# Optimization experiments

Measured on AMD Instinct MI355X. Metric: run time of the kernel, lower is better.

## Reference

```python
import jax, jax.numpy as jnp
import numpy as np
from jax import lax

GRID_SIZE = 5
SPLINE_ORDER = 3
N_COEF = GRID_SIZE + SPLINE_ORDER  # 8 b-spline basis functions per input
GRID_LO, GRID_HI = -1.0, 1.0


def _grid():
    h = (GRID_HI - GRID_LO) / GRID_SIZE
    return jnp.arange(-SPLINE_ORDER, GRID_SIZE + SPLINE_ORDER + 1, dtype=jnp.float32) * h + GRID_LO


def _bsplines(x):
    # x: [..., in] -> [..., in, N_COEF] via Cox-de Boor recursion (efficient-kan)
    grid = _grid()
    x = x[..., None]
    bases = ((x >= grid[:-1]) & (x < grid[1:])).astype(x.dtype)
    for j in range(1, SPLINE_ORDER + 1):
        bases = ((x - grid[:-(j + 1)]) / (grid[j:-1] - grid[:-(j + 1)]) * bases[..., :-1]
                 + (grid[j + 1:] - x) / (grid[j + 1:] - grid[1:-j]) * bases[..., 1:])
    return bases


def _kan_linear(x, base_w, spline_w):
    # x: [..., in]; base_w: [out, in]; spline_w: [out, in, N_COEF]
    base = jax.nn.silu(x) @ base_w.T
    b = _bsplines(x).reshape(x.shape[:-1] + (-1,))  # [..., in*N_COEF]
    return base + b @ spline_w.reshape(spline_w.shape[0], -1).T


def _kan_conv(x, base_w, spline_w):
    # x: [B, C, H, W]; 3x3 valid KAN convolution
    patches = lax.conv_general_dilated_patches(x, (3, 3), (1, 1), 'VALID')  # [B, C*9, H-2, W-2]
    p = patches.transpose(0, 2, 3, 1)  # [B, Ho, Wo, C*9]
    out = _kan_linear(p, base_w, spline_w)  # [B, Ho, Wo, out]
    return out.transpose(0, 3, 1, 2)


def _maxpool2(x):
    return lax.reduce_window(x, -jnp.inf, lax.max, (1, 1, 2, 2), (1, 1, 2, 2), 'VALID')


def setup_inputs() -> dict:
    key = jax.random.key(0)
    ks = jax.random.split(key, 12)
    B = 2048
    x = jax.random.uniform(ks[0], (B, 1, 28, 28), dtype=jnp.float32)
    s = 0.1
    return {
        'x': x,
        'bw1': jax.random.normal(ks[1], (5, 9), dtype=jnp.float32) * s,
        'sw1': jax.random.normal(ks[2], (5, 9, N_COEF), dtype=jnp.float32) * s,
        'bw2': jax.random.normal(ks[3], (5, 45), dtype=jnp.float32) * s,
        'sw2': jax.random.normal(ks[4], (5, 45, N_COEF), dtype=jnp.float32) * s,
        'bw3': jax.random.normal(ks[5], (2, 45), dtype=jnp.float32) * s,
        'sw3': jax.random.normal(ks[6], (2, 45, N_COEF), dtype=jnp.float32) * s,
        'w1': jax.random.normal(ks[7], (500, 162), dtype=jnp.float32) * 0.05,
        'b1': jnp.zeros((500,), dtype=jnp.float32),
        'w2': jax.random.normal(ks[8], (10, 500), dtype=jnp.float32) * 0.05,
        'b2': jnp.zeros((10,), dtype=jnp.float32),
    }


def reference(x, bw1, sw1, bw2, sw2, bw3, sw3, w1, b1, w2, b2):
    h = _kan_conv(x, bw1, sw1)       # [B, 5, 26, 26]
    h = _maxpool2(h)                 # [B, 5, 13, 13]
    h = _kan_conv(h, bw2, sw2)       # [B, 5, 11, 11]
    h = _kan_conv(h, bw3, sw3)       # [B, 2, 9, 9]
    h = h.reshape(h.shape[0], -1)    # [B, 162]
    h = jax.nn.relu(h @ w1.T + b1)   # [B, 500]
    return h @ w2.T + b2             # [B, 10]
```

## Files before the change

### kernel.cpp

```cpp
#include <hip/hip_runtime.h>


typedef _Float16 h2 __attribute__((ext_vector_type(2)));

__device__ __forceinline__ h2 u2h(unsigned int u) {
  union { unsigned int x; h2 h; } v; v.x = u; return v.h;
}
__device__ __forceinline__ unsigned short f2h_bits(float x) {
  union { _Float16 h; unsigned short u; } v; v.h = (_Float16)x; return v.u;
}
__device__ __forceinline__ unsigned int pack2h(float a, float b) {
  return (unsigned int)f2h_bits(a) | ((unsigned int)f2h_bits(b) << 16);
}
__device__ __forceinline__ float fdot2(h2 a, h2 b, float c) {
  return __builtin_amdgcn_fdot2(a, b, c, false);
}

__device__ __forceinline__ void featurize_regs(float v, uint4& bs, float& silu) {
  silu = v / (1.0f + __expf(-v));
  bs.x = 0u; bs.y = 0u; bs.z = 0u; bs.w = 0u;
  float u = fmaf(v, 2.5f, 5.5f);
  if (u >= 0.0f && u < 11.0f) {
    float tf = floorf(u);
    float f = u - tf, f2 = f * f, f3 = f2 * f, om = 1.0f - f;
    const float c6 = 1.0f / 6.0f;
    float w0 = om * om * om * c6;
    float w1 = (3.0f * f3 - 6.0f * f2 + 4.0f) * c6;
    float w2 = (-3.0f * f3 + 3.0f * f2 + 3.0f * f + 1.0f) * c6;
    float w3 = f3 * c6;
    unsigned long long w01 =
        (unsigned long long)f2h_bits(w0) |
        ((unsigned long long)f2h_bits(w1) << 16) |
        ((unsigned long long)f2h_bits(w2) << 32) |
        ((unsigned long long)f2h_bits(w3) << 48);
    int t = (int)tf;
    int s = 16 * t - 48;
    unsigned long long lo, hi;
    if (s >= 0) {
      lo = (s < 64) ? (w01 << s) : 0ull;
      hi = (s == 0) ? 0ull : ((s < 64) ? (w01 >> (64 - s)) : (w01 << (s - 64)));
    } else {
      lo = w01 >> (-s);
      hi = 0ull;
    }
    bs.x = (unsigned int)lo; bs.y = (unsigned int)(lo >> 32);
    bs.z = (unsigned int)hi; bs.w = (unsigned int)(hi >> 32);
  }
}

__global__ __launch_bounds__(256) void k_prep(
    const float* __restrict__ bw1, const float* __restrict__ sw1,
    const float* __restrict__ bw2, const float* __restrict__ sw2,
    const float* __restrict__ bw3, const float* __restrict__ sw3,
    const float* __restrict__ w1,
    unsigned int* __restrict__ V1s, float* __restrict__ V1b,
    unsigned int* __restrict__ V2s, float* __restrict__ V2b,
    unsigned int* __restrict__ V3s, float* __restrict__ V3b,
    unsigned int* __restrict__ W1p) {
  int t = blockIdx.x * 256 + threadIdx.x;
  if (t < 180) {
    int p = t & 3, o = (t >> 2) % 5, in = t / 20;
    V1s[t] = pack2h(sw1[(o * 9 + in) * 8 + 2 * p], sw1[(o * 9 + in) * 8 + 2 * p + 1]);
  }
  if (t < 45)  { int o = t % 5, in = t / 5; V1b[t] = bw1[o * 9 + in]; }
  if (t < 900) {
    int p = t & 3, o = (t >> 2) % 5, in = t / 20;
    V2s[t] = pack2h(sw2[(o * 45 + in) * 8 + 2 * p], sw2[(o * 45 + in) * 8 + 2 * p + 1]);
  }
  if (t < 225) { int o = t % 5, in = t / 5; V2b[t] = bw2[o * 45 + in]; }
  if (t < 360) {
    int p = t & 3, o = (t >> 2) & 1, in = t / 8;
    V3s[t] = pack2h(sw3[(o * 45 + in) * 8 + 2 * p], sw3[(o * 45 + in) * 8 + 2 * p + 1]);
  }
  if (t < 90)  { int o = t % 2, in = t / 2; V3b[t] = bw3[o * 45 + in]; }
  if (t < 81 * 512) {
    int kp = t >> 9, o = t & 511;
    W1p[t] = (o < 500) ? pack2h(w1[o * 162 + 2 * kp], w1[o * 162 + 2 * kp + 1]) : 0u;
  }
}

__global__ __launch_bounds__(256) void k_fused(
    const float* __restrict__ x,
    const unsigned int* __restrict__ V1s, const float* __restrict__ V1b,
    const unsigned int* __restrict__ V2s, const float* __restrict__ V2b,
    const unsigned int* __restrict__ V3s, const float* __restrict__ V3b,
    const unsigned int* __restrict__ W1p,
    const float* __restrict__ b1,
    const float* __restrict__ W2, const float* __restrict__ b2,
    float* __restrict__ out) {
  __shared__ uint4 bas[845];
  __shared__ float ext[845];
  __shared__ float hbuf[845];
  __shared__ unsigned int hpk[81];
  const int b = blockIdx.x;
  const int tid = threadIdx.x;

  for (int l = tid; l < 784; l += 256) {
    uint4 bs; float sl;
    featurize_regs(x[b * 784 + l], bs, sl);
    bas[l] = bs; ext[l] = sl;
  }
  __syncthreads();

  if (tid < 169) {
    int py = tid / 13, px = tid % 13;
    int r0 = py * 2, c0 = px * 2;
    float wacc[4][5];
    #pragma unroll
    for (int wi = 0; wi < 4; ++wi)
      #pragma unroll
      for (int o = 0; o < 5; ++o) wacc[wi][o] = 0.0f;
    #pragma unroll
    for (int r = 0; r < 4; ++r) {
      #pragma unroll
      for (int c = 0; c < 4; ++c) {
        uint4 q = bas[(r0 + r) * 28 + c0 + c];
        float sl = ext[(r0 + r) * 28 + c0 + c];
        h2 a0 = u2h(q.x), a1 = u2h(q.y), a2 = u2h(q.z), a3 = u2h(q.w);
        #pragma unroll
        for (int dy = 0; dy < 2; ++dy) {
          #pragma unroll
          for (int dx = 0; dx < 2; ++dx) {
            int ky = r - dy, kx = c - dx;
            if (ky >= 0 && ky < 3 && kx >= 0 && kx < 3) {
              const unsigned int* wp = V1s + (ky * 3 + kx) * 20;
              const float* bp = V1b + (ky * 3 + kx) * 5;
              #pragma unroll
              for (int o = 0; o < 5; ++o) {
                float acc = wacc[dy * 2 + dx][o];
                acc = fdot2(a0, u2h(wp[o * 4 + 0]), acc);
                acc = fdot2(a1, u2h(wp[o * 4 + 1]), acc);
                acc = fdot2(a2, u2h(wp[o * 4 + 2]), acc);
                acc = fdot2(a3, u2h(wp[o * 4 + 3]), acc);
                wacc[dy * 2 + dx][o] = fmaf(sl, bp[o], acc);
              }
            }
          }
        }
      }
    }
    #pragma unroll
    for (int o = 0; o < 5; ++o) {
      float m = fmaxf(fmaxf(wacc[0][o], wacc[1][o]), fmaxf(wacc[2][o], wacc[3][o]));
      hbuf[o * 169 + tid] = m;
    }
  }
  __syncthreads();

  for (int l = tid; l < 845; l += 256) {
    uint4 bs; float sl;
    featurize_regs(hbuf[l], bs, sl);
    bas[l] = bs; ext[l] = sl;
  }
  __syncthreads();

  if (tid < 121) {
    int y = tid / 11, xx = tid % 11;
    float acc[5] = {0.f, 0.f, 0.f, 0.f, 0.f};
    #pragma unroll 1
    for (int cky = 0; cky < 15; ++cky) {
      int c = cky / 3, ky = cky % 3;
      int base = c * 169 + (y + ky) * 13 + xx;
      #pragma unroll
      for (int kx = 0; kx < 3; ++kx) {
        uint4 q = bas[base + kx];
        float sl = ext[base + kx];
        h2 a0 = u2h(q.x), a1 = u2h(q.y), a2 = u2h(q.z), a3 = u2h(q.w);
        const unsigned int* wp = V2s + (cky * 3 + kx) * 20;
        const float* bp = V2b + (cky * 3 + kx) * 5;
        #pragma unroll
        for (int o = 0; o < 5; ++o) {
          float a = acc[o];
          a = fdot2(a0, u2h(wp[o * 4 + 0]), a);
          a = fdot2(a1, u2h(wp[o * 4 + 1]), a);
          a = fdot2(a2, u2h(wp[o * 4 + 2]), a);
          a = fdot2(a3, u2h(wp[o * 4 + 3]), a);
          acc[o] = fmaf(sl, bp[o], a);
        }
      }
    }
    #pragma unroll
    for (int o = 0; o < 5; ++o) hbuf[o * 121 + tid] = acc[o];
  }
  __syncthreads();

  for (int l = tid; l < 605; l += 256) {
    uint4 bs; float sl;
    featurize_regs(hbuf[l], bs, sl);
    bas[l] = bs; ext[l] = sl;
  }
  __syncthreads();

  if (tid < 81) {
    int y = tid / 9, xx = tid % 9;
    float acc[2] = {0.f, 0.f};
    #pragma unroll 1
    for (int cky = 0; cky < 15; ++cky) {
      int c = cky / 3, ky = cky % 3;
      int base = c * 121 + (y + ky) * 11 + xx;
      #pragma unroll
      for (int kx = 0; kx < 3; ++kx) {
        uint4 q = bas[base + kx];
        float sl = ext[base + kx];
        h2 a0 = u2h(q.x), a1 = u2h(q.y), a2 = u2h(q.z), a3 = u2h(q.w);
        const unsigned int* wp = V3s + (cky * 3 + kx) * 8;
        const float* bp = V3b + (cky * 3 + kx) * 2;
        #pragma unroll
        for (int o = 0; o < 2; ++o) {
          float a = acc[o];
          a = fdot2(a0, u2h(wp[o * 4 + 0]), a);
          a = fdot2(a1, u2h(wp[o * 4 + 1]), a);
          a = fdot2(a2, u2h(wp[o * 4 + 2]), a);
          a = fdot2(a3, u2h(wp[o * 4 + 3]), a);
          acc[o] = fmaf(sl, bp[o], a);
        }
      }
    }
    hbuf[tid] = acc[0];
    hbuf[81 + tid] = acc[1];
  }
  __syncthreads();

  if (tid < 81) hpk[tid] = pack2h(hbuf[2 * tid], hbuf[2 * tid + 1]);
  __syncthreads();

  if (tid < 250) {
    float a0 = 0.0f, a1 = 0.0f;
    #pragma unroll 4
    for (int kp = 0; kp < 81; ++kp) {
      h2 hk = u2h(hpk[kp]);
      uint2 wv = *(const uint2*)(W1p + kp * 512 + 2 * tid);
      a0 = fdot2(hk, u2h(wv.x), a0);
      a1 = fdot2(hk, u2h(wv.y), a1);
    }
    int o0 = 2 * tid, o1 = 2 * tid + 1;
    float v0 = a0 + b1[o0], v1 = a1 + b1[o1];
    hbuf[200 + o0] = v0 > 0.0f ? v0 : 0.0f;
    hbuf[200 + o1] = v1 > 0.0f ? v1 : 0.0f;
  }
  __syncthreads();

  if (tid < 160) {
    int o = tid >> 4, part = tid & 15;
    float s = 0.0f;
    #pragma unroll
    for (int j = 0; j < 8; ++j) {
      int k = part * 4 + j * 64;
      if (k <= 496) {
        float4 w = *(const float4*)&W2[o * 500 + k];
        float4 h = *(const float4*)&hbuf[200 + k];
        s += w.x * h.x + w.y * h.y + w.z * h.z + w.w * h.w;
      }
    }
    hbuf[tid] = s;
  }
  __syncthreads();

  if (tid < 10) {
    float s = 0.0f;
    #pragma unroll
    for (int p = 0; p < 16; ++p) s += hbuf[tid * 16 + p];
    out[b * 10 + tid] = s + b2[tid];
  }
}

extern "C" void kernel_launch(void* const* d_in, const int* in_sizes, int n_in,
                              void* d_out, int out_size, void* d_ws, size_t ws_size,
                              hipStream_t stream) {
  (void)in_sizes; (void)n_in; (void)out_size; (void)ws_size;
  const float* x   = (const float*)d_in[0];
  const float* bw1 = (const float*)d_in[1];
  const float* sw1 = (const float*)d_in[2];
  const float* bw2 = (const float*)d_in[3];
  const float* sw2 = (const float*)d_in[4];
  const float* bw3 = (const float*)d_in[5];
  const float* sw3 = (const float*)d_in[6];
  const float* w1  = (const float*)d_in[7];
  const float* b1  = (const float*)d_in[8];
  const float* w2  = (const float*)d_in[9];
  const float* b2  = (const float*)d_in[10];
  float* out = (float*)d_out;

  char* ws = (char*)d_ws;
  unsigned int* V1s = (unsigned int*)(ws);
  float*        V1b = (float*)(ws + 768);
  unsigned int* V2s = (unsigned int*)(ws + 1024);
  float*        V2b = (float*)(ws + 4672);
  unsigned int* V3s = (unsigned int*)(ws + 5632);
  float*        V3b = (float*)(ws + 7168);
  unsigned int* W1p = (unsigned int*)(ws + 7680);

  k_prep<<<162, 256, 0, stream>>>(bw1, sw1, bw2, sw2, bw3, sw3, w1,
                                  V1s, V1b, V2s, V2b, V3s, V3b, W1p);
  k_fused<<<2048, 256, 0, stream>>>(x, V1s, V1b, V2s, V2b, V3s, V3b, W1p,
                                    b1, w2, b2, out);
}
```

Measured before the change: 141.0 us.

## Rebalance conv stages: per-pixel conv1 with separate pool, split-K conv2/conv3 across waves

Conv1 now computes each of the 676 output pixels once, with all threads participating, and stores them as fp16 in scratch. A separate pass then max-pools and featurizes, replacing the old scheme where 169 threads each computed a 2x2 window with redundant loads. Conv2 and conv3 split the input-channel/ky reduction across two wave parities so more threads are active. Partial sums are combined through scratch during the following featurize/pack step. This costs extra shared memory, an fp16 rounding of conv1 outputs before pooling, and an additional reduction step.

```diff
diff --git a/kernel.cpp b/kernel.cpp
--- a/kernel.cpp
+++ b/kernel.cpp
@@ -90,10 +90,14 @@
     float* __restrict__ out) {
   __shared__ uint4 bas[845];
   __shared__ float ext[845];
-  __shared__ float hbuf[845];
-  __shared__ unsigned int hpk[81];
+  __shared__ float hbuf[700];
+  __shared__ float scratch[1690];
+  unsigned short* co  = (unsigned short*)scratch;
+  unsigned int*  co32 = (unsigned int*)scratch;
+  unsigned int*  hpk  = (unsigned int*)ext;
   const int b = blockIdx.x;
   const int tid = threadIdx.x;
+  const int wv = tid >> 6, lane = tid & 63;
 
   for (int l = tid; l < 784; l += 256) {
     uint4 bs; float sl;
@@ -102,72 +106,19 @@
   }
   __syncthreads();
 
-  if (tid < 169) {
-    int py = tid / 13, px = tid % 13;
-    int r0 = py * 2, c0 = px * 2;
-    float wacc[4][5];
+  for (int l = tid; l < 676; l += 256) {
+    int y = l / 26, xx = l % 26;
+    float acc[5] = {0.f, 0.f, 0.f, 0.f, 0.f};
     #pragma unroll
-    for (int wi = 0; wi < 4; ++wi)
-      #pragma unroll
-      for (int o = 0; o < 5; ++o) wacc[wi][o] = 0.0f;
-    #pragma unroll
-    for (int r = 0; r < 4; ++r) {
-      #pragma unroll
-      for (int c = 0; c < 4; ++c) {
-        uint4 q = bas[(r0 + r) * 28 + c0 + c];
-        float sl = ext[(r0 + r) * 28 + c0 + c];
-        h2 a0 = u2h(q.x), a1 = u2h(q.y), a2 = u2h(q.z), a3 = u2h(q.w);
-        #pragma unroll
-        for (int dy = 0; dy < 2; ++dy) {
-          #pragma unroll
-          for (int dx = 0; dx < 2; ++dx) {
-            int ky = r - dy, kx = c - dx;
-            if (ky >= 0 && ky < 3 && kx >= 0 && kx < 3) {
-              const unsigned int* wp = V1s + (ky * 3 + kx) * 20;
-              const float* bp = V1b + (ky * 3 + kx) * 5;
-              #pragma unroll
-              for (int o = 0; o < 5; ++o) {
-                float acc = wacc[dy * 2 + dx][o];
-                acc = fdot2(a0, u2h(wp[o * 4 + 0]), acc);
-                acc = fdot2(a1, u2h(wp[o * 4 + 1]), acc);
-                acc = fdot2(a2, u2h(wp[o * 4 + 2]), acc);
-                acc = fdot2(a3, u2h(wp[o * 4 + 3]), acc);
-                wacc[dy * 2 + dx][o] = fmaf(sl, bp[o], acc);
-              }
-            }
-          }
-        }
-      }
-    }
-    #pragma unroll
-    for (int o = 0; o < 5; ++o) {
-      float m = fmaxf(fmaxf(wacc[0][o], wacc[1][o]), fmaxf(wacc[2][o], wacc[3][o]));
-      hbuf[o * 169 + tid] = m;
-    }
-  }
-  __syncthreads();
-
-  for (int l = tid; l < 845; l += 256) {
-    uint4 bs; float sl;
-    featurize_regs(hbuf[l], bs, sl);
-    bas[l] = bs; ext[l] = sl;
-  }
-  __syncthreads();
-
-  if (tid < 121) {
-    int y = tid / 11, xx = tid % 11;
-    float acc[5] = {0.f, 0.f, 0.f, 0.f, 0.f};
-    #pragma unroll 1
-    for (int cky = 0; cky < 15; ++cky) {
-      int c = cky / 3, ky = cky % 3;
-      int base = c * 169 + (y + ky) * 13 + xx;
+    for (int ky = 0; ky < 3; ++ky) {
       #pragma unroll
       for (int kx = 0; kx < 3; ++kx) {
-        uint4 q = bas[base + kx];
-        float sl = ext[base + kx];
+        int r = (y + ky) * 28 + xx + kx;
+        uint4 q = bas[r];
+        float sl = ext[r];
         h2 a0 = u2h(q.x), a1 = u2h(q.y), a2 = u2h(q.z), a3 = u2h(q.w);
-        const unsigned int* wp = V2s + (cky * 3 + kx) * 20;
-        const float* bp = V2b + (cky * 3 + kx) * 5;
+        const unsigned int* wp = V1s + (ky * 3 + kx) * 20;
+        const float* bp = V1b + (ky * 3 + kx) * 5;
         #pragma unroll
         for (int o = 0; o < 5; ++o) {
           float a = acc[o];
@@ -180,48 +131,106 @@
       }
     }
     #pragma unroll
-    for (int o = 0; o < 5; ++o) hbuf[o * 121 + tid] = acc[o];
-  }
-  __syncthreads();
-
-  for (int l = tid; l < 605; l += 256) {
+    for (int o = 0; o < 5; ++o) co[o * 676 + l] = f2h_bits(acc[o]);
+  }
+  __syncthreads();
+
+  for (int l = tid; l < 845; l += 256) {
+    int o = l / 169, p = l % 169;
+    int py = p / 13, px = p % 13;
+    int base = o * 338 + py * 26 + px;
+    h2 r0 = u2h(co32[base]);
+    h2 r1 = u2h(co32[base + 13]);
+    float m = fmaxf(fmaxf((float)r0.x, (float)r0.y),
+                    fmaxf((float)r1.x, (float)r1.y));
     uint4 bs; float sl;
-    featurize_regs(hbuf[l], bs, sl);
+    featurize_regs(m, bs, sl);
     bas[l] = bs; ext[l] = sl;
   }
   __syncthreads();
 
-  if (tid < 81) {
-    int y = tid / 9, xx = tid % 9;
-    float acc[2] = {0.f, 0.f};
-    #pragma unroll 1
-    for (int cky = 0; cky < 15; ++cky) {
-      int c = cky / 3, ky = cky % 3;
-      int base = c * 121 + (y + ky) * 11 + xx;
-      #pragma unroll
-      for (int kx = 0; kx < 3; ++kx) {
-        uint4 q = bas[base + kx];
-        float sl = ext[base + kx];
-        h2 a0 = u2h(q.x), a1 = u2h(q.y), a2 = u2h(q.z), a3 = u2h(q.w);
-        const unsigned int* wp = V3s + (cky * 3 + kx) * 8;
-        const float* bp = V3b + (cky * 3 + kx) * 2;
+  {
+    int par = wv & 1;
+    int pos = (wv >> 1) * 64 + lane;
+    if (pos < 121) {
+      int y = pos / 11, xx = pos % 11;
+      float acc[5] = {0.f, 0.f, 0.f, 0.f, 0.f};
+      #pragma unroll 1
+      for (int cky = par; cky < 15; cky += 2) {
+        int c = cky / 3, ky = cky % 3;
+        int base = c * 169 + (y + ky) * 13 + xx;
         #pragma unroll
-        for (int o = 0; o < 2; ++o) {
-          float a = acc[o];
-          a = fdot2(a0, u2h(wp[o * 4 + 0]), a);
-          a = fdot2(a1, u2h(wp[o * 4 + 1]), a);
-          a = fdot2(a2, u2h(wp[o * 4 + 2]), a);
-          a = fdot2(a3, u2h(wp[o * 4 + 3]), a);
-          acc[o] = fmaf(sl, bp[o], a);
+        for (int kx = 0; kx < 3; ++kx) {
+          uint4 q = bas[base + kx];
+          float sl = ext[base + kx];
+          h2 a0 = u2h(q.x), a1 = u2h(q.y), a2 = u2h(q.z), a3 = u2h(q.w);
+          const unsigned int* wp = V2s + (cky * 3 + kx) * 20;
+          const float* bp = V2b + (cky * 3 + kx) * 5;
+          #pragma unroll
+          for (int o = 0; o < 5; ++o) {
+            float a = acc[o];
+            a = fdot2(a0, u2h(wp[o * 4 + 0]), a);
+            a = fdot2(a1, u2h(wp[o * 4 + 1]), a);
+            a = fdot2(a2, u2h(wp[o * 4 + 2]), a);
+            a = fdot2(a3, u2h(wp[o * 4 + 3]), a);
+            acc[o] = fmaf(sl, bp[o], a);
+          }
         }
       }
-    }
-    hbuf[tid] = acc[0];
-    hbuf[81 + tid] = acc[1];
-  }
-  __syncthreads();
-
-  if (tid < 81) hpk[tid] = pack2h(hbuf[2 * tid], hbuf[2 * tid + 1]);
+      #pragma unroll
+      for (int o = 0; o < 5; ++o)
+        scratch[par * 605 + o * 121 + pos] = acc[o];
+    }
+  }
+  __syncthreads();
+
+  for (int l = tid; l < 605; l += 256) {
+    float v = scratch[l] + scratch[605 + l];
+    uint4 bs; float sl;
+    featurize_regs(v, bs, sl);
+    bas[l] = bs; ext[l] = sl;
+  }
+  __syncthreads();
+
+  {
+    int par = wv & 1;
+    int pos = (wv >> 1) * 64 + lane;
+    if (pos < 81) {
+      int y = pos / 9, xx = pos % 9;
+      float acc[2] = {0.f, 0.f};
+      #pragma unroll 1
+      for (int cky = par; cky < 15; cky += 2) {
+        int c = cky / 3, ky = cky % 3;
+        int base = c * 121 + (y + ky) * 11 + xx;
+        #pragma unroll
+        for (int kx = 0; kx < 3; ++kx) {
+          uint4 q = bas[base + kx];
+          float sl = ext[base + kx];
+          h2 a0 = u2h(q.x), a1 = u2h(q.y), a2 = u2h(q.z), a3 = u2h(q.w);
+          const unsigned int* wp = V3s + (cky * 3 + kx) * 8;
+          const float* bp = V3b + (cky * 3 + kx) * 2;
+          #pragma unroll
+          for (int o = 0; o < 2; ++o) {
+            float a = acc[o];
+            a = fdot2(a0, u2h(wp[o * 4 + 0]), a);
+            a = fdot2(a1, u2h(wp[o * 4 + 1]), a);
+            a = fdot2(a2, u2h(wp[o * 4 + 2]), a);
+            a = fdot2(a3, u2h(wp[o * 4 + 3]), a);
+            acc[o] = fmaf(sl, bp[o], a);
+          }
+        }
+      }
+      scratch[par * 162 + pos]      = acc[0];
+      scratch[par * 162 + 81 + pos] = acc[1];
+    }
+  }
+  __syncthreads();
+
+  if (tid < 81) {
+    float s0 = scratch[2 * tid]     + scratch[162 + 2 * tid];
+    float s1 = scratch[2 * tid + 1] + scratch[162 + 2 * tid + 1];
+    hpk[tid] = pack2h(s0, s1);
+  }
   __syncthreads();
 
   if (tid < 250) {
@@ -229,9 +238,9 @@
     #pragma unroll 4
     for (int kp = 0; kp < 81; ++kp) {
       h2 hk = u2h(hpk[kp]);
-      uint2 wv = *(const uint2*)(W1p + kp * 512 + 2 * tid);
-      a0 = fdot2(hk, u2h(wv.x), a0);
-      a1 = fdot2(hk, u2h(wv.y), a1);
+      uint2 wvv = *(const uint2*)(W1p + kp * 512 + 2 * tid);
+      a0 = fdot2(hk, u2h(wvv.x), a0);
+      a1 = fdot2(hk, u2h(wvv.y), a1);
     }
     int o0 = 2 * tid, o1 = 2 * tid + 1;
     float v0 = a0 + b1[o0], v1 = a1 + b1[o1];
```

New measurement: 159.9 us. 13.4% more time.
